# Kernel tuning notes

Hardware: AMD Instinct MI355X
Metric: run time of the kernel (lower is better)

Reference implementation:

```python
import jax, jax.numpy as jnp
import numpy as np

B, C, H, W = 8, 16, 128, 128
P = H * W            # pixel_number = 16384
KN = 16              # kernel_number_per_pixel
CK = C * 9           # in_channel * kernel_size = 144


def setup_inputs() -> dict:
    key = jax.random.key(0)
    k1, k2, k3 = jax.random.split(key, 3)
    x = jax.random.normal(k1, (B, C, H, W), dtype=jnp.float32)
    weights = jax.random.normal(k2, (P, KN, CK), dtype=jnp.float32)
    hash_idx = jax.random.randint(k3, (P, CK), 0, C * H * W, dtype=jnp.int64)
    return {"x": x, "weights": weights, "hash_idx": hash_idx}


def reference(x, weights, hash_idx):
    b, c, h, w = x.shape
    img_size = c * h * w
    flat = x.reshape(-1)  # [B*C*H*W]
    # per-batch offset of the per-pixel hash table (torch fallback branch)
    idx = hash_idx[None, :, :] + (jnp.arange(b, dtype=hash_idx.dtype) * img_size)[:, None, None]  # [B,P,CK]
    patches = flat[idx]  # [B, P, CK] hash-indexed gather (im2col)
    # weights [P,KN,CK] @ patches [P,CK,B] -> [P,KN,B]; transpose(0,2) -> [B,KN,P]
    return jnp.einsum('pkc,bpc->bkp', weights, patches)
```

## Files before the change

kernel.cpp:

```cpp
#include <hip/hip_runtime.h>
#include <hip/hip_bf16.h>

#define P_TOTAL 16384
#define KN      16
#define CK      144
#define BATCH   8
#define IMG     262144
#define PSTRIDE 12

__global__ __launch_bounds__(256) void transpose_x_bf16(
    const float* __restrict__ x, float4* __restrict__ xt)
{
    const int i = blockIdx.x * 256 + threadIdx.x;
    union { __hip_bfloat16 h[8]; float4 f4; } u;
#pragma unroll
    for (int b = 0; b < BATCH; ++b)
        u.h[b] = __float2bfloat16(
            __builtin_nontemporal_load(&x[(size_t)b * IMG + i]));
    xt[i] = u.f4;
}

__global__ __launch_bounds__(256) void abc2d_xt(
    const float4* __restrict__ xt,
    const float*  __restrict__ w,
    const int*    __restrict__ hidx,
    float* __restrict__ out)
{
    __shared__ float patch[CK * PSTRIDE];

    const int bid = blockIdx.x;
    const int p   = (bid & 7) * (P_TOTAL / 8) + (bid >> 3);
    const int t   = threadIdx.x;
    const int k   = t >> 4;
    const int cs  = t & 15;

    const bool do_g = (t < CK);
    float4 g;
    if (do_g) {
        const int id = __builtin_nontemporal_load(&hidx[p * CK + t]);
        g = xt[id];
    }

    const float* wp = w + (size_t)p * (KN * CK) + (size_t)k * CK;
    float wreg[9];
#pragma unroll
    for (int i = 0; i < 9; ++i)
        wreg[i] = __builtin_nontemporal_load(&wp[cs + 16 * i]);

    if (do_g) {
        union { __hip_bfloat16 h[8]; float4 f4; } u;
        u.f4 = g;
        float* pr = &patch[t * PSTRIDE];
        *reinterpret_cast<float4*>(pr) = make_float4(
            __bfloat162float(u.h[0]), __bfloat162float(u.h[1]),
            __bfloat162float(u.h[2]), __bfloat162float(u.h[3]));
        *reinterpret_cast<float4*>(pr + 4) = make_float4(
            __bfloat162float(u.h[4]), __bfloat162float(u.h[5]),
            __bfloat162float(u.h[6]), __bfloat162float(u.h[7]));
    }
    __syncthreads();

    float acc[BATCH];
#pragma unroll
    for (int b = 0; b < BATCH; ++b) acc[b] = 0.f;

#pragma unroll
    for (int i = 0; i < 9; ++i) {
        const int c = cs + 16 * i;
        const float wv = wreg[i];
        const float* pr = &patch[c * PSTRIDE];
        const float4 p0 = *reinterpret_cast<const float4*>(pr);
        const float4 p1 = *reinterpret_cast<const float4*>(pr + 4);
        acc[0] += wv * p0.x;
        acc[1] += wv * p0.y;
        acc[2] += wv * p0.z;
        acc[3] += wv * p0.w;
        acc[4] += wv * p1.x;
        acc[5] += wv * p1.y;
        acc[6] += wv * p1.z;
        acc[7] += wv * p1.w;
    }

#pragma unroll
    for (int b = 0; b < BATCH; ++b) {
        float v = acc[b];
        v += __shfl_xor(v, 1);
        v += __shfl_xor(v, 2);
        v += __shfl_xor(v, 4);
        v += __shfl_xor(v, 8);
        acc[b] = v;
    }

    if (cs == 0) {
#pragma unroll
        for (int b = 0; b < BATCH; ++b)
            __builtin_nontemporal_store(
                acc[b], &out[(size_t)b * (KN * P_TOTAL) + (size_t)k * P_TOTAL + p]);
    }
}

__global__ __launch_bounds__(256) void abc2d_direct(
    const float* __restrict__ x, const float* __restrict__ w,
    const int* __restrict__ hidx, float* __restrict__ out)
{
    __shared__ float patch[CK * PSTRIDE];
    const int bid = blockIdx.x;
    const int p   = (bid & 7) * (P_TOTAL / 8) + (bid >> 3);
    const int t   = threadIdx.x;
    const int k   = t >> 4;
    const int cs  = t & 15;

    if (t < CK) {
        const int id = hidx[p * CK + t];
        float v[BATCH];
#pragma unroll
        for (int b = 0; b < BATCH; ++b) v[b] = x[(size_t)b * IMG + (size_t)id];
        float* pr = &patch[t * PSTRIDE];
        *reinterpret_cast<float4*>(pr)     = make_float4(v[0], v[1], v[2], v[3]);
        *reinterpret_cast<float4*>(pr + 4) = make_float4(v[4], v[5], v[6], v[7]);
    }

    const float* wp = w + (size_t)p * (KN * CK) + (size_t)k * CK;
    float wreg[9];
#pragma unroll
    for (int i = 0; i < 9; ++i) wreg[i] = wp[cs + 16 * i];
    __syncthreads();

    float acc[BATCH];
#pragma unroll
    for (int b = 0; b < BATCH; ++b) acc[b] = 0.f;
#pragma unroll
    for (int i = 0; i < 9; ++i) {
        const float wv = wreg[i];
        const float* pr = &patch[(cs + 16 * i) * PSTRIDE];
        const float4 p0 = *reinterpret_cast<const float4*>(pr);
        const float4 p1 = *reinterpret_cast<const float4*>(pr + 4);
        acc[0] += wv * p0.x; acc[1] += wv * p0.y; acc[2] += wv * p0.z; acc[3] += wv * p0.w;
        acc[4] += wv * p1.x; acc[5] += wv * p1.y; acc[6] += wv * p1.z; acc[7] += wv * p1.w;
    }
#pragma unroll
    for (int b = 0; b < BATCH; ++b) {
        float v = acc[b];
        v += __shfl_xor(v, 1); v += __shfl_xor(v, 2);
        v += __shfl_xor(v, 4); v += __shfl_xor(v, 8);
        acc[b] = v;
    }
    if (cs == 0) {
#pragma unroll
        for (int b = 0; b < BATCH; ++b)
            out[(size_t)b * (KN * P_TOTAL) + (size_t)k * P_TOTAL + p] = acc[b];
    }
}

extern "C" void kernel_launch(void* const* d_in, const int* in_sizes, int n_in,
                              void* d_out, int out_size, void* d_ws, size_t ws_size,
                              hipStream_t stream) {
    const float* x    = (const float*)d_in[0];
    const float* wts  = (const float*)d_in[1];
    const int*   hidx = (const int*)d_in[2];
    float* out = (float*)d_out;

    const size_t xt_bytes = (size_t)IMG * BATCH * sizeof(__hip_bfloat16);
    if (ws_size >= xt_bytes) {
        float4* xt = (float4*)d_ws;
        transpose_x_bf16<<<IMG / 256, 256, 0, stream>>>(x, xt);
        abc2d_xt<<<P_TOTAL, 256, 0, stream>>>(xt, wts, hidx, out);
    } else {
        abc2d_direct<<<P_TOTAL, 256, 0, stream>>>(x, wts, hidx, out);
    }
}
```

Before: 250.3 us.

## Process eight pixels per block with double-buffered gather and weight prefetch

```diff
diff --git a/kernel.cpp b/kernel.cpp
--- a/kernel.cpp
+++ b/kernel.cpp
@@ -7,6 +7,9 @@
 #define BATCH   8
 #define IMG     262144
 #define PSTRIDE 12
+#define NP      8
+#define NCHUNK  (P_TOTAL / NP)
+
 
 __global__ __launch_bounds__(256) void transpose_x_bf16(
     const float* __restrict__ x, float4* __restrict__ xt)
@@ -20,82 +23,121 @@
     xt[i] = u.f4;
 }
 
-__global__ __launch_bounds__(256) void abc2d_xt(
+__global__ __launch_bounds__(256) void abc2d_xt_pipe(
     const float4* __restrict__ xt,
     const float*  __restrict__ w,
     const int*    __restrict__ hidx,
     float* __restrict__ out)
 {
-    __shared__ float patch[CK * PSTRIDE];
-
-    const int bid = blockIdx.x;
-    const int p   = (bid & 7) * (P_TOTAL / 8) + (bid >> 3);
-    const int t   = threadIdx.x;
-    const int k   = t >> 4;
-    const int cs  = t & 15;
-
+    __shared__ float patch[2][CK * PSTRIDE];
+    __shared__ float outbuf[KN * BATCH * NP];
+
+    const int bid   = blockIdx.x;
+    const int chunk = (bid & 7) * (NCHUNK / 8) + (bid >> 3);
+    const int p0    = chunk * NP;
+    const int t     = threadIdx.x;
+    const int k     = t >> 4;
+    const int cs    = t & 15;
     const bool do_g = (t < CK);
+
+    float wcur[9], wnxt[9];
     float4 g;
+    int id_nxt = 0;
+
+    {
+        const float* wp = w + (size_t)p0 * (KN * CK) + (size_t)k * CK + cs;
+#pragma unroll
+        for (int i = 0; i < 9; ++i)
+            wcur[i] = __builtin_nontemporal_load(wp + 16 * i);
+    }
     if (do_g) {
-        const int id = __builtin_nontemporal_load(&hidx[p * CK + t]);
-        g = xt[id];
-    }
-
-    const float* wp = w + (size_t)p * (KN * CK) + (size_t)k * CK;
-    float wreg[9];
-#pragma unroll
-    for (int i = 0; i < 9; ++i)
-        wreg[i] = __builtin_nontemporal_load(&wp[cs + 16 * i]);
-
-    if (do_g) {
-        union { __hip_bfloat16 h[8]; float4 f4; } u;
-        u.f4 = g;
-        float* pr = &patch[t * PSTRIDE];
-        *reinterpret_cast<float4*>(pr) = make_float4(
-            __bfloat162float(u.h[0]), __bfloat162float(u.h[1]),
-            __bfloat162float(u.h[2]), __bfloat162float(u.h[3]));
-        *reinterpret_cast<float4*>(pr + 4) = make_float4(
-            __bfloat162float(u.h[4]), __bfloat162float(u.h[5]),
-            __bfloat162float(u.h[6]), __bfloat162float(u.h[7]));
-    }
+        const int id0 = hidx[p0 * CK + t];
+        g = xt[id0];
+        id_nxt = hidx[(p0 + 1) * CK + t];
+    }
+
+#pragma unroll
+    for (int j = 0; j < NP; ++j) {
+        const int jb = j & 1;
+
+        if (j + 1 < NP) {
+            const float* wp = w + (size_t)(p0 + j + 1) * (KN * CK) + (size_t)k * CK + cs;
+#pragma unroll
+            for (int i = 0; i < 9; ++i)
+                wnxt[i] = __builtin_nontemporal_load(wp + 16 * i);
+        }
+
+        if (do_g) {
+            union { __hip_bfloat16 h[8]; float4 f4; } u;
+            u.f4 = g;
+            float* pr = &patch[jb][t * PSTRIDE];
+            *reinterpret_cast<float4*>(pr) = make_float4(
+                __bfloat162float(u.h[0]), __bfloat162float(u.h[1]),
+                __bfloat162float(u.h[2]), __bfloat162float(u.h[3]));
+            *reinterpret_cast<float4*>(pr + 4) = make_float4(
+                __bfloat162float(u.h[4]), __bfloat162float(u.h[5]),
+                __bfloat162float(u.h[6]), __bfloat162float(u.h[7]));
+        }
+        __syncthreads();
+
+        if (do_g && j + 1 < NP) {
+            g = xt[id_nxt];
+            if (j + 2 < NP) id_nxt = hidx[(p0 + j + 2) * CK + t];
+        }
+
+        float acc[BATCH];
+#pragma unroll
+        for (int b = 0; b < BATCH; ++b) acc[b] = 0.f;
+
+#pragma unroll
+        for (int i = 0; i < 9; ++i) {
+            const int c = cs + 16 * i;
+            const float wv = wcur[i];
+            const float* pr = &patch[jb][c * PSTRIDE];
+            const float4 q0 = *reinterpret_cast<const float4*>(pr);
+            const float4 q1 = *reinterpret_cast<const float4*>(pr + 4);
+            acc[0] += wv * q0.x;
+            acc[1] += wv * q0.y;
+            acc[2] += wv * q0.z;
+            acc[3] += wv * q0.w;
+            acc[4] += wv * q1.x;
+            acc[5] += wv * q1.y;
+            acc[6] += wv * q1.z;
+            acc[7] += wv * q1.w;
+        }
+
+#pragma unroll
+        for (int b = 0; b < BATCH; ++b) {
+            float v = acc[b];
+            v += __shfl_xor(v, 1);
+            v += __shfl_xor(v, 2);
+            v += __shfl_xor(v, 4);
+            v += __shfl_xor(v, 8);
+            acc[b] = v;
+        }
+
+        if (cs == 0) {
+#pragma unroll
+            for (int b = 0; b < BATCH; ++b)
+                outbuf[(k * BATCH + b) * NP + j] = acc[b];
+        }
+
+        if (j + 1 < NP) {
+#pragma unroll
+            for (int i = 0; i < 9; ++i) wcur[i] = wnxt[i];
+        }
+    }
+
     __syncthreads();
-
-    float acc[BATCH];
-#pragma unroll
-    for (int b = 0; b < BATCH; ++b) acc[b] = 0.f;
-
-#pragma unroll
-    for (int i = 0; i < 9; ++i) {
-        const int c = cs + 16 * i;
-        const float wv = wreg[i];
-        const float* pr = &patch[c * PSTRIDE];
-        const float4 p0 = *reinterpret_cast<const float4*>(pr);
-        const float4 p1 = *reinterpret_cast<const float4*>(pr + 4);
-        acc[0] += wv * p0.x;
-        acc[1] += wv * p0.y;
-        acc[2] += wv * p0.z;
-        acc[3] += wv * p0.w;
-        acc[4] += wv * p1.x;
-        acc[5] += wv * p1.y;
-        acc[6] += wv * p1.z;
-        acc[7] += wv * p1.w;
-    }
-
-#pragma unroll
-    for (int b = 0; b < BATCH; ++b) {
-        float v = acc[b];
-        v += __shfl_xor(v, 1);
-        v += __shfl_xor(v, 2);
-        v += __shfl_xor(v, 4);
-        v += __shfl_xor(v, 8);
-        acc[b] = v;
-    }
-
-    if (cs == 0) {
-#pragma unroll
-        for (int b = 0; b < BATCH; ++b)
-            __builtin_nontemporal_store(
-                acc[b], &out[(size_t)b * (KN * P_TOTAL) + (size_t)k * P_TOTAL + p]);
+    if (t < KN * BATCH) {
+        const int kk = t >> 3;
+        const int bb = t & 7;
+        const float* src = &outbuf[(kk * BATCH + bb) * NP];
+        const float4 v0 = *reinterpret_cast<const float4*>(src);
+        const float4 v1 = *reinterpret_cast<const float4*>(src + 4);
+        float* dst = &out[((size_t)bb * KN + kk) * P_TOTAL + p0];
+        *reinterpret_cast<float4*>(dst)     = v0;
+        *reinterpret_cast<float4*>(dst + 4) = v1;
     }
 }
 
@@ -133,10 +175,10 @@
     for (int i = 0; i < 9; ++i) {
         const float wv = wreg[i];
         const float* pr = &patch[(cs + 16 * i) * PSTRIDE];
-        const float4 p0 = *reinterpret_cast<const float4*>(pr);
-        const float4 p1 = *reinterpret_cast<const float4*>(pr + 4);
-        acc[0] += wv * p0.x; acc[1] += wv * p0.y; acc[2] += wv * p0.z; acc[3] += wv * p0.w;
-        acc[4] += wv * p1.x; acc[5] += wv * p1.y; acc[6] += wv * p1.z; acc[7] += wv * p1.w;
+        const float4 q0 = *reinterpret_cast<const float4*>(pr);
+        const float4 q1 = *reinterpret_cast<const float4*>(pr + 4);
+        acc[0] += wv * q0.x; acc[1] += wv * q0.y; acc[2] += wv * q0.z; acc[3] += wv * q0.w;
+        acc[4] += wv * q1.x; acc[5] += wv * q1.y; acc[6] += wv * q1.z; acc[7] += wv * q1.w;
     }
 #pragma unroll
     for (int b = 0; b < BATCH; ++b) {
@@ -164,7 +206,7 @@
     if (ws_size >= xt_bytes) {
         float4* xt = (float4*)d_ws;
         transpose_x_bf16<<<IMG / 256, 256, 0, stream>>>(x, xt);
-        abc2d_xt<<<P_TOTAL, 256, 0, stream>>>(xt, wts, hidx, out);
+        abc2d_xt_pipe<<<NCHUNK, 256, 0, stream>>>(xt, wts, hidx, out);
     } else {
         abc2d_direct<<<P_TOTAL, 256, 0, stream>>>(x, wts, hidx, out);
     }
```

Result: faster. 235.4 us (-6.0%).
